# Kernel tuning notes

Hardware: AMD Instinct MI355X
Metric: run time of the kernel (lower is better)

Reference implementation:

```python
import jax, jax.numpy as jnp
import numpy as np

INPUT_DIM = 512
N_CLASSES = 100
N_SUBNETS = 20
HIDDEN = 32
WS1 = INPUT_DIM * HIDDEN   # 16384
BS1 = HIDDEN               # 32
WS2 = HIDDEN * N_CLASSES   # 3200
BS2 = N_CLASSES            # 100
TOTAL = WS1 + BS1 + WS2 + BS2  # 19716
LN_EPS = 1e-5


def _layernorm(v, g, b):
    mu = jnp.mean(v, axis=-1, keepdims=True)
    var = jnp.mean(jnp.square(v - mu), axis=-1, keepdims=True)
    return (v - mu) * jax.lax.rsqrt(var + LN_EPS) * g + b


def setup_inputs() -> dict:
    key = jax.random.key(0)
    ks = jax.random.split(key, 12)
    def lin(k, fan_in, shape):
        bound = 1.0 / np.sqrt(fan_in)
        return jax.random.uniform(k, shape, jnp.float32, -bound, bound)
    return {
        "x": jax.random.normal(ks[0], (32768, INPUT_DIM), jnp.float32),
        "W_h1": lin(ks[1], INPUT_DIM, (128, INPUT_DIM)),
        "b_h1": lin(ks[2], INPUT_DIM, (128,)),
        "g1": jnp.ones((128,), jnp.float32),
        "be1": jnp.zeros((128,), jnp.float32),
        "W_h2": lin(ks[3], 128, (256, 128)),
        "b_h2": lin(ks[4], 128, (256,)),
        "g2": jnp.ones((256,), jnp.float32),
        "be2": jnp.zeros((256,), jnp.float32),
        "W_h3": lin(ks[5], 256, (N_SUBNETS * TOTAL, 256)),
        "b_h3": lin(ks[6], 256, (N_SUBNETS * TOTAL,)),
        "ens_w": jnp.full((N_SUBNETS,), 1.0 / N_SUBNETS, jnp.float32),
    }


def reference(x, W_h1, b_h1, g1, be1, W_h2, b_h2, g2, be2, W_h3, b_h3, ens_w):
    # context from support set (= x itself): (1, input_dim)
    context = jnp.mean(x, axis=0, keepdims=True)
    # hypernet MLP (eval mode: dropout = identity)
    h = jax.nn.relu(_layernorm(context @ W_h1.T + b_h1, g1, be1))
    h = jax.nn.relu(_layernorm(h @ W_h2.T + b_h2, g2, be2))
    all_params = (h @ W_h3.T + b_h3).reshape(N_SUBNETS, TOTAL)
    # split generated params (same layout as torch .view)
    W1 = all_params[:, :WS1].reshape(N_SUBNETS, HIDDEN, INPUT_DIM)       # (S,H,I)
    b1 = all_params[:, WS1:WS1 + BS1]                                     # (S,H)
    W2 = all_params[:, WS1 + BS1:WS1 + BS1 + WS2].reshape(N_SUBNETS, N_CLASSES, HIDDEN)  # (S,C,H)
    b2 = all_params[:, WS1 + BS1 + WS2:]                                  # (S,C)
    # batched per-subnet 2-layer nets (dropout p=0.2 is identity in eval)
    hh = jax.nn.relu(jnp.einsum('bi,shi->sbh', x, W1) + b1[:, None, :])   # (S,B,H)
    logits = jnp.einsum('sbh,sch->sbc', hh, W2) + b2[:, None, :]          # (S,B,C)
    w = jax.nn.softmax(ens_w)                                             # (S,)
    return jnp.einsum('s,sbc->bc', w, logits)                             # (B,C)
```

## Files before the change

kernel.cpp:

```cpp
#include <hip/hip_runtime.h>
#include <hip/hip_bf16.h>

#define BATCH   32768
#define DIM     512
#define H1N     128
#define H2N     256
#define NSUB    20
#define HID     32
#define NCLS    100
#define NHID    640
#define TOTALP  19716
#define NPAR    394320
#define WS1P    16384
#define WS1B1   16416
#define WS2END  19616

#define OFF_PART 0
#define OFF_H    262144
#define OFF_W    262400
#define OFF_B1   262432
#define OFF_B2R  263072
#define OFF_W1B  265072
#define OFF_W2B  428912
#define OFF_XB   469872

typedef __attribute__((ext_vector_type(8))) short short8;
typedef __attribute__((ext_vector_type(4))) float f32x4;

static __device__ inline unsigned short f2bf(float f) {
    __hip_bfloat16 h = __float2bfloat16(f);
    return *reinterpret_cast<unsigned short*>(&h);
}

static __device__ __forceinline__ void gload16(const void* g, void* l) {
    __builtin_amdgcn_global_load_lds(
        (const __attribute__((address_space(1))) void*)g,
        (__attribute__((address_space(3))) void*)l, 16, 0, 0);
}

__global__ __launch_bounds__(256) void k1_colsum(const float* __restrict__ x,
                                                 float* __restrict__ F) {
    __shared__ float sP[DIM];
    int t = threadIdx.x, bid = blockIdx.x;
    int par = t >> 7;
    int c4 = (t & 127) * 4;
    const float* xb = x + (size_t)bid * 64 * DIM;
    unsigned short* ob = (unsigned short*)(F + OFF_XB) + (size_t)bid * 64 * DIM;
    float4 acc = make_float4(0.f, 0.f, 0.f, 0.f);
    #pragma unroll 8
    for (int i = 0; i < 32; ++i) {
        int r = 2 * i + par;
        float4 v = *(const float4*)(xb + r * DIM + c4);
        acc.x += v.x; acc.y += v.y; acc.z += v.z; acc.w += v.w;
        ushort4 u;
        u.x = f2bf(v.x); u.y = f2bf(v.y); u.z = f2bf(v.z); u.w = f2bf(v.w);
        *(ushort4*)(ob + r * DIM + c4) = u;
    }
    if (par == 0) *(float4*)(sP + c4) = acc;
    __syncthreads();
    if (par == 1) {
        float4 p = *(const float4*)(sP + c4);
        p.x += acc.x; p.y += acc.y; p.z += acc.z; p.w += acc.w;
        *(float4*)(F + OFF_PART + bid * DIM + c4) = p;
    }
}

__global__ __launch_bounds__(256) void k2_hyper(
    const float* __restrict__ Wh1, const float* __restrict__ bh1,
    const float* __restrict__ g1,  const float* __restrict__ be1,
    const float* __restrict__ Wh2, const float* __restrict__ bh2,
    const float* __restrict__ g2,  const float* __restrict__ be2,
    const float* __restrict__ ensw, float* __restrict__ F)
{
    __shared__ __align__(16) float sctx[DIM];
    __shared__ __align__(16) float sP2[DIM];
    __shared__ __align__(16) float sh1[H1N];
    __shared__ __align__(16) float sh2[H2N];
    int t = threadIdx.x;

    {
        int c4 = (t & 127) * 4;
        int half = t >> 7;
        float4 a = make_float4(0.f, 0.f, 0.f, 0.f);
        #pragma unroll 8
        for (int b = half * 256; b < half * 256 + 256; ++b) {
            float4 v = *(const float4*)(F + OFF_PART + b * DIM + c4);
            a.x += v.x; a.y += v.y; a.z += v.z; a.w += v.w;
        }
        if (half == 0) *(float4*)(sP2 + c4) = a;
        __syncthreads();
        if (half == 1) {
            float4 o = *(const float4*)(sP2 + c4);
            o.x = (o.x + a.x) * (1.0f / BATCH);
            o.y = (o.y + a.y) * (1.0f / BATCH);
            o.z = (o.z + a.z) * (1.0f / BATCH);
            o.w = (o.w + a.w) * (1.0f / BATCH);
            *(float4*)(sctx + c4) = o;
        }
        __syncthreads();
    }

    if (t < H1N) {
        float v = bh1[t];
        const float4* w = (const float4*)(Wh1 + t * DIM);
        for (int k = 0; k < DIM / 4; ++k) {
            float4 ww = w[k]; float4 c = *(const float4*)(sctx + k * 4);
            v += ww.x * c.x + ww.y * c.y + ww.z * c.z + ww.w * c.w;
        }
        sh1[t] = v;
    }
    __syncthreads();
    {
        float mu = 0.f;
        for (int k = 0; k < H1N; ++k) mu += sh1[k];
        mu *= (1.0f / H1N);
        float var = 0.f;
        for (int k = 0; k < H1N; ++k) { float d = sh1[k] - mu; var += d * d; }
        var *= (1.0f / H1N);
        float inv = rsqrtf(var + 1e-5f);
        __syncthreads();
        if (t < H1N) {
            float v = (sh1[t] - mu) * inv * g1[t] + be1[t];
            sh1[t] = fmaxf(v, 0.f);
        }
        __syncthreads();
    }

    {
        float v = bh2[t];
        const float4* w = (const float4*)(Wh2 + t * H1N);
        for (int k = 0; k < H1N / 4; ++k) {
            float4 ww = w[k]; float4 c = *(const float4*)(sh1 + k * 4);
            v += ww.x * c.x + ww.y * c.y + ww.z * c.z + ww.w * c.w;
        }
        sh2[t] = v;
    }
    __syncthreads();
    {
        float mu = 0.f;
        for (int k = 0; k < H2N; ++k) mu += sh2[k];
        mu *= (1.0f / H2N);
        float var = 0.f;
        for (int k = 0; k < H2N; ++k) { float d = sh2[k] - mu; var += d * d; }
        var *= (1.0f / H2N);
        float inv = rsqrtf(var + 1e-5f);
        float v = (sh2[t] - mu) * inv * g2[t] + be2[t];
        F[OFF_H + t] = fmaxf(v, 0.f);
    }

    if (t == 0) {
        float m = -1e30f;
        for (int s = 0; s < NSUB; ++s) m = fmaxf(m, ensw[s]);
        float sum = 0.f, e[NSUB];
        for (int s = 0; s < NSUB; ++s) { e[s] = __expf(ensw[s] - m); sum += e[s]; }
        for (int s = 0; s < NSUB; ++s) F[OFF_W + s] = e[s] / sum;
    }
}

static __device__ __forceinline__ void k3_pack(float* F, int row, float val) {
    __hip_bfloat16* W1B = (__hip_bfloat16*)(F + OFF_W1B);
    __hip_bfloat16* W2B = (__hip_bfloat16*)(F + OFF_W2B);
    int s = row / TOTALP;
    int r = row - s * TOTALP;
    if (r < WS1P) {
        int hh = r >> 9, k = r & 511;
        W1B[(s * HID + hh) * DIM + k] = __float2bfloat16(val);
    } else if (r < WS1B1) {
        F[OFF_B1 + s * HID + (r - WS1P)] = val;
    } else if (r < WS2END) {
        int q = r - WS1B1; int c = q >> 5, hh = q & 31;
        float ws = F[OFF_W + s];
        W2B[c * NHID + s * HID + hh] = __float2bfloat16(ws * val);
    } else {
        F[OFF_B2R + s * NCLS + (r - WS2END)] = val;
    }
}

__global__ __launch_bounds__(256) void k3_gemv(
    const float* __restrict__ Wh3, const float* __restrict__ bh3, float* __restrict__ F)
{
    int t = threadIdx.x;
    int wid = t >> 6, lane = t & 63;
    int row0 = blockIdx.x * 8 + wid * 2;
    const float4 h = *(const float4*)(F + OFF_H + lane * 4);
    const float4 w0 = *(const float4*)(Wh3 + (size_t)row0 * 256 + lane * 4);
    const float4 w1 = *(const float4*)(Wh3 + (size_t)(row0 + 1) * 256 + lane * 4);
    float d0 = w0.x * h.x + w0.y * h.y + w0.z * h.z + w0.w * h.w;
    float d1 = w1.x * h.x + w1.y * h.y + w1.z * h.z + w1.w * h.w;
    #pragma unroll
    for (int off = 32; off; off >>= 1) {
        d0 += __shfl_down(d0, off);
        d1 += __shfl_down(d1, off);
    }
    if (lane == 0) {
        k3_pack(F, row0,     d0 + bh3[row0]);
        k3_pack(F, row0 + 1, d1 + bh3[row0 + 1]);
    }
}

__global__ __launch_bounds__(256) void gemm_fused(
    const __hip_bfloat16* __restrict__ XB, const __hip_bfloat16* __restrict__ W1B,
    const __hip_bfloat16* __restrict__ W2B, const float* __restrict__ F,
    float* __restrict__ out)
{
    __shared__ __align__(16) unsigned char sA[64 * 256];
    __shared__ __align__(16) unsigned char sB[128 * 256];
    __shared__ __align__(16) unsigned char sP[64 * 256];
    const int t = threadIdx.x;
    int bid = blockIdx.x;
    const int cpx = gridDim.x >> 3;
    bid = (bid & 7) * cpx + (bid >> 3);
    const int Row0 = bid * 64;
    const int wid = t >> 6, lane = t & 63;
    const int l16 = lane & 15, lq = lane >> 4;

    f32x4 acc2[8];
    #pragma unroll
    for (int fn = 0; fn < 8; ++fn) acc2[fn] = (f32x4){0.f, 0.f, 0.f, 0.f};

    for (int n1 = 0; n1 < 5; ++n1) {
        f32x4 acc1[8];
        #pragma unroll
        for (int fn = 0; fn < 8; ++fn) acc1[fn] = (f32x4){0.f, 0.f, 0.f, 0.f};

        for (int kc = 0; kc < 512; kc += 128) {
            __syncthreads();
            #pragma unroll
            for (int i = 0; i < 4; ++i) {
                int ul = (wid * 4 + i) * 64 + lane;
                int row = ul >> 4, u = ul & 15;
                gload16(XB + (size_t)(Row0 + row) * 512 + kc + ((u ^ (row & 7)) << 3),
                        sA + (wid * 4 + i) * 1024);
            }
            #pragma unroll
            for (int i = 0; i < 8; ++i) {
                int ul = (wid * 8 + i) * 64 + lane;
                int row = ul >> 4, u = ul & 15;
                gload16(W1B + (size_t)(n1 * 128 + row) * 512 + kc + ((u ^ (row & 7)) << 3),
                        sB + (wid * 8 + i) * 1024);
            }
            __syncthreads();
            #pragma unroll
            for (int kk = 0; kk < 4; ++kk) {
                int u = kk * 4 + lq;
                int arow = wid * 16 + l16;
                short8 af = *(const short8*)(sA + arow * 256 + ((u ^ (arow & 7)) << 4));
                short8 bfv[8];
                #pragma unroll
                for (int fn = 0; fn < 8; ++fn) {
                    int rw = fn * 16 + l16;
                    bfv[fn] = *(const short8*)(sB + rw * 256 + ((u ^ (rw & 7)) << 4));
                }
                #pragma unroll
                for (int fn = 0; fn < 8; ++fn)
                    acc1[fn] = __builtin_amdgcn_mfma_f32_16x16x32_bf16(
                        af, bfv[fn], acc1[fn], 0, 0, 0);
            }
        }

        #pragma unroll
        for (int fn = 0; fn < 8; ++fn) {
            int col = fn * 16 + l16;
            float b1v = F[OFF_B1 + n1 * 128 + col];
            int unit = col >> 3;
            #pragma unroll
            for (int r = 0; r < 4; ++r) {
                int row = wid * 16 + lq * 4 + r;
                float v = fmaxf(acc1[fn][r] + b1v, 0.f);
                *(unsigned short*)(sP + row * 256 + ((unit ^ (row & 7)) << 4)
                                   + (col & 7) * 2) = f2bf(v);
            }
        }

        __syncthreads();
        #pragma unroll
        for (int i = 0; i < 8; ++i) {
            int ul = (wid * 8 + i) * 64 + lane;
            int row = ul >> 4, u = ul & 15;
            gload16(W2B + (size_t)row * NHID + n1 * 128 + ((u ^ (row & 7)) << 3),
                    sB + (wid * 8 + i) * 1024);
        }
        __syncthreads();
        #pragma unroll
        for (int kk = 0; kk < 4; ++kk) {
            int u = kk * 4 + lq;
            int arow = wid * 16 + l16;
            short8 af = *(const short8*)(sP + arow * 256 + ((u ^ (arow & 7)) << 4));
            short8 bfv[8];
            #pragma unroll
            for (int fn = 0; fn < 8; ++fn) {
                int rw = fn * 16 + l16;
                bfv[fn] = *(const short8*)(sB + rw * 256 + ((u ^ (rw & 7)) << 4));
            }
            #pragma unroll
            for (int fn = 0; fn < 8; ++fn)
                acc2[fn] = __builtin_amdgcn_mfma_f32_16x16x32_bf16(
                    af, bfv[fn], acc2[fn], 0, 0, 0);
        }
    }

    float* sBe = (float*)sA;
    __syncthreads();
    if (t < 128) {
        float b = 0.f;
        if (t < NCLS) {
            #pragma unroll
            for (int s = 0; s < NSUB; ++s)
                b += F[OFF_W + s] * F[OFF_B2R + s * NCLS + t];
        }
        sBe[t] = b;
    }
    __syncthreads();

    #pragma unroll
    for (int fn = 0; fn < 8; ++fn) {
        int gcol = fn * 16 + l16;
        if (gcol < NCLS) {
            float be = sBe[gcol];
            #pragma unroll
            for (int r = 0; r < 4; ++r) {
                int grow = Row0 + wid * 16 + lq * 4 + r;
                out[(size_t)grow * NCLS + gcol] = acc2[fn][r] + be;
            }
        }
    }
}

extern "C" void kernel_launch(void* const* d_in, const int* in_sizes, int n_in,
                              void* d_out, int out_size, void* d_ws, size_t ws_size,
                              hipStream_t stream)
{
    const float* x    = (const float*)d_in[0];
    const float* Wh1  = (const float*)d_in[1];
    const float* bh1  = (const float*)d_in[2];
    const float* g1   = (const float*)d_in[3];
    const float* be1  = (const float*)d_in[4];
    const float* Wh2  = (const float*)d_in[5];
    const float* bh2  = (const float*)d_in[6];
    const float* g2   = (const float*)d_in[7];
    const float* be2  = (const float*)d_in[8];
    const float* Wh3  = (const float*)d_in[9];
    const float* bh3  = (const float*)d_in[10];
    const float* ensw = (const float*)d_in[11];
    float* F = (float*)d_ws;
    float* out = (float*)d_out;

    const __hip_bfloat16* XB  = (const __hip_bfloat16*)(F + OFF_XB);
    const __hip_bfloat16* W1B = (const __hip_bfloat16*)(F + OFF_W1B);
    const __hip_bfloat16* W2B = (const __hip_bfloat16*)(F + OFF_W2B);

    k1_colsum<<<512, 256, 0, stream>>>(x, F);
    k2_hyper<<<1, 256, 0, stream>>>(Wh1, bh1, g1, be1, Wh2, bh2, g2, be2, ensw, F);
    k3_gemv<<<NPAR / 8, 256, 0, stream>>>(Wh3, bh3, F);
    gemm_fused<<<BATCH / 64, 256, 0, stream>>>(XB, W1B, W2B, F, out);
}
```

Before: 193.8 us.

## Double-buffer LDS tiles and switch to a 2x2 warp layout in the fused GEMM

Restructures the fused two-GEMM kernel into a flat 50-phase software pipeline. K-chunks are halved to 64 and the A/B LDS tiles are double-buffered, so the global loads for the next phase are issued while the current phase computes, with one barrier per phase instead of two. Warps are rearranged from a 4x1 layout (16 rows by 128 columns) to a 2x2 layout (32 rows by 64 columns), which cuts redundant B-fragment LDS reads per MFMA. In exchange it runs more, smaller phases with more control logic, and the per-phase lambda branches may add register pressure.

```diff
diff --git a/kernel.cpp b/kernel.cpp
--- a/kernel.cpp
+++ b/kernel.cpp
@@ -203,8 +203,8 @@
     const __hip_bfloat16* __restrict__ W2B, const float* __restrict__ F,
     float* __restrict__ out)
 {
-    __shared__ __align__(16) unsigned char sA[64 * 256];
-    __shared__ __align__(16) unsigned char sB[128 * 256];
+    __shared__ __align__(16) unsigned char sA[2][64 * 128];
+    __shared__ __align__(16) unsigned char sB[2][128 * 128];
     __shared__ __align__(16) unsigned char sP[64 * 256];
     const int t = threadIdx.x;
     int bid = blockIdx.x;
@@ -213,94 +213,140 @@
     const int Row0 = bid * 64;
     const int wid = t >> 6, lane = t & 63;
     const int l16 = lane & 15, lq = lane >> 4;
-
-    f32x4 acc2[8];
+    const int wr = wid >> 1, wc = wid & 1;
+
+    f32x4 acc1[2][4], acc2[2][4];
     #pragma unroll
-    for (int fn = 0; fn < 8; ++fn) acc2[fn] = (f32x4){0.f, 0.f, 0.f, 0.f};
-
-    for (int n1 = 0; n1 < 5; ++n1) {
-        f32x4 acc1[8];
+    for (int fm = 0; fm < 2; ++fm)
         #pragma unroll
-        for (int fn = 0; fn < 8; ++fn) acc1[fn] = (f32x4){0.f, 0.f, 0.f, 0.f};
-
-        for (int kc = 0; kc < 512; kc += 128) {
-            __syncthreads();
+        for (int fn = 0; fn < 4; ++fn)
+            acc2[fm][fn] = (f32x4){0.f, 0.f, 0.f, 0.f};
+
+    auto stage = [&](int p, int b) {
+        int n1 = p / 10, ph = p - n1 * 10;
+        if (ph < 8) {
+            int kc = ph * 64;
+            #pragma unroll
+            for (int i = 0; i < 2; ++i) {
+                int cidx = wid * 2 + i;
+                int ul = cidx * 64 + lane;
+                int row = ul >> 3, u = ul & 7;
+                gload16(XB + (size_t)(Row0 + row) * 512 + kc + ((u ^ (row & 7)) << 3),
+                        &sA[b][cidx * 1024]);
+            }
             #pragma unroll
             for (int i = 0; i < 4; ++i) {
-                int ul = (wid * 4 + i) * 64 + lane;
-                int row = ul >> 4, u = ul & 15;
-                gload16(XB + (size_t)(Row0 + row) * 512 + kc + ((u ^ (row & 7)) << 3),
-                        sA + (wid * 4 + i) * 1024);
-            }
-            #pragma unroll
-            for (int i = 0; i < 8; ++i) {
-                int ul = (wid * 8 + i) * 64 + lane;
-                int row = ul >> 4, u = ul & 15;
+                int cidx = wid * 4 + i;
+                int ul = cidx * 64 + lane;
+                int row = ul >> 3, u = ul & 7;
                 gload16(W1B + (size_t)(n1 * 128 + row) * 512 + kc + ((u ^ (row & 7)) << 3),
-                        sB + (wid * 8 + i) * 1024);
-            }
-            __syncthreads();
-            #pragma unroll
-            for (int kk = 0; kk < 4; ++kk) {
-                int u = kk * 4 + lq;
-                int arow = wid * 16 + l16;
-                short8 af = *(const short8*)(sA + arow * 256 + ((u ^ (arow & 7)) << 4));
-                short8 bfv[8];
-                #pragma unroll
-                for (int fn = 0; fn < 8; ++fn) {
-                    int rw = fn * 16 + l16;
-                    bfv[fn] = *(const short8*)(sB + rw * 256 + ((u ^ (rw & 7)) << 4));
-                }
-                #pragma unroll
-                for (int fn = 0; fn < 8; ++fn)
-                    acc1[fn] = __builtin_amdgcn_mfma_f32_16x16x32_bf16(
-                        af, bfv[fn], acc1[fn], 0, 0, 0);
-            }
-        }
-
+                        &sB[b][cidx * 1024]);
+            }
+        } else {
+            int h = ph - 8;
+            #pragma unroll
+            for (int i = 0; i < 4; ++i) {
+                int cidx = wid * 4 + i;
+                int ul = cidx * 64 + lane;
+                int row = ul >> 3, u = ul & 7;
+                gload16(W2B + (size_t)row * NHID + n1 * 128 + h * 64 + ((u ^ (row & 7)) << 3),
+                        &sB[b][cidx * 1024]);
+            }
+        }
+    };
+
+    auto compute = [&](int p, int b) {
+        int n1 = p / 10, ph = p - n1 * 10;
+        if (ph < 8) {
+            #pragma unroll
+            for (int kkl = 0; kkl < 2; ++kkl) {
+                int u = kkl * 4 + lq;
+                short8 af[2], bfv[4];
+                #pragma unroll
+                for (int fm = 0; fm < 2; ++fm) {
+                    int arow = wr * 32 + fm * 16 + l16;
+                    af[fm] = *(const short8*)(&sA[b][arow * 128 + ((u ^ (arow & 7)) << 4)]);
+                }
+                #pragma unroll
+                for (int fn = 0; fn < 4; ++fn) {
+                    int brow = wc * 64 + fn * 16 + l16;
+                    bfv[fn] = *(const short8*)(&sB[b][brow * 128 + ((u ^ (brow & 7)) << 4)]);
+                }
+                #pragma unroll
+                for (int fm = 0; fm < 2; ++fm)
+                    #pragma unroll
+                    for (int fn = 0; fn < 4; ++fn)
+                        acc1[fm][fn] = __builtin_amdgcn_mfma_f32_16x16x32_bf16(
+                            af[fm], bfv[fn], acc1[fm][fn], 0, 0, 0);
+            }
+        } else {
+            int h = ph - 8;
+            #pragma unroll
+            for (int kkl = 0; kkl < 2; ++kkl) {
+                int u = kkl * 4 + lq;
+                int punit = (h * 2 + kkl) * 4 + lq;
+                short8 af[2], bfv[4];
+                #pragma unroll
+                for (int fm = 0; fm < 2; ++fm) {
+                    int prow = wr * 32 + fm * 16 + l16;
+                    af[fm] = *(const short8*)(&sP[prow * 256 + ((punit ^ (prow & 7)) << 4)]);
+                }
+                #pragma unroll
+                for (int fn = 0; fn < 4; ++fn) {
+                    int brow = wc * 64 + fn * 16 + l16;
+                    bfv[fn] = *(const short8*)(&sB[b][brow * 128 + ((u ^ (brow & 7)) << 4)]);
+                }
+                #pragma unroll
+                for (int fm = 0; fm < 2; ++fm)
+                    #pragma unroll
+                    for (int fn = 0; fn < 4; ++fn)
+                        acc2[fm][fn] = __builtin_amdgcn_mfma_f32_16x16x32_bf16(
+                            af[fm], bfv[fn], acc2[fm][fn], 0, 0, 0);
+            }
+        }
+    };
+
+    auto pack = [&](int n1) {
         #pragma unroll
-        for (int fn = 0; fn < 8; ++fn) {
-            int col = fn * 16 + l16;
-            float b1v = F[OFF_B1 + n1 * 128 + col];
-            int unit = col >> 3;
-            #pragma unroll
-            for (int r = 0; r < 4; ++r) {
-                int row = wid * 16 + lq * 4 + r;
-                float v = fmaxf(acc1[fn][r] + b1v, 0.f);
-                *(unsigned short*)(sP + row * 256 + ((unit ^ (row & 7)) << 4)
-                                   + (col & 7) * 2) = f2bf(v);
-            }
-        }
-
+        for (int fm = 0; fm < 2; ++fm) {
+            #pragma unroll
+            for (int fn = 0; fn < 4; ++fn) {
+                int col = wc * 64 + fn * 16 + l16;
+                float b1v = F[OFF_B1 + n1 * 128 + col];
+                int unit = col >> 3;
+                #pragma unroll
+                for (int r = 0; r < 4; ++r) {
+                    int row = wr * 32 + fm * 16 + lq * 4 + r;
+                    float v = fmaxf(acc1[fm][fn][r] + b1v, 0.f);
+                    *(unsigned short*)(&sP[row * 256 + ((unit ^ (row & 7)) << 4)
+                                       + (col & 7) * 2]) = f2bf(v);
+                }
+            }
+        }
+    };
+
+    stage(0, 0);
+    __syncthreads();
+    int buf = 0;
+    for (int p = 0; p < 49; ++p) {
+        stage(p + 1, buf ^ 1);
+        int ph = p % 10;
+        if (ph == 0) {
+            #pragma unroll
+            for (int fm = 0; fm < 2; ++fm)
+                #pragma unroll
+                for (int fn = 0; fn < 4; ++fn)
+                    acc1[fm][fn] = (f32x4){0.f, 0.f, 0.f, 0.f};
+        }
+        compute(p, buf);
+        if (ph == 7) pack(p / 10);
         __syncthreads();
-        #pragma unroll
-        for (int i = 0; i < 8; ++i) {
-            int ul = (wid * 8 + i) * 64 + lane;
-            int row = ul >> 4, u = ul & 15;
-            gload16(W2B + (size_t)row * NHID + n1 * 128 + ((u ^ (row & 7)) << 3),
-                    sB + (wid * 8 + i) * 1024);
-        }
-        __syncthreads();
-        #pragma unroll
-        for (int kk = 0; kk < 4; ++kk) {
-            int u = kk * 4 + lq;
-            int arow = wid * 16 + l16;
-            short8 af = *(const short8*)(sP + arow * 256 + ((u ^ (arow & 7)) << 4));
-            short8 bfv[8];
-            #pragma unroll
-            for (int fn = 0; fn < 8; ++fn) {
-                int rw = fn * 16 + l16;
-                bfv[fn] = *(const short8*)(sB + rw * 256 + ((u ^ (rw & 7)) << 4));
-            }
-            #pragma unroll
-            for (int fn = 0; fn < 8; ++fn)
-                acc2[fn] = __builtin_amdgcn_mfma_f32_16x16x32_bf16(
-                    af, bfv[fn], acc2[fn], 0, 0, 0);
-        }
-    }
-
-    float* sBe = (float*)sA;
-    __syncthreads();
+        buf ^= 1;
+    }
+    compute(49, buf);
+    __syncthreads();
+
+    float* sBe = (float*)&sA[0][0];
     if (t < 128) {
         float b = 0.f;
         if (t < NCLS) {
@@ -313,14 +359,17 @@
     __syncthreads();
 
     #pragma unroll
-    for (int fn = 0; fn < 8; ++fn) {
-        int gcol = fn * 16 + l16;
-        if (gcol < NCLS) {
-            float be = sBe[gcol];
-            #pragma unroll
-            for (int r = 0; r < 4; ++r) {
-                int grow = Row0 + wid * 16 + lq * 4 + r;
-                out[(size_t)grow * NCLS + gcol] = acc2[fn][r] + be;
+    for (int fm = 0; fm < 2; ++fm) {
+        #pragma unroll
+        for (int fn = 0; fn < 4; ++fn) {
+            int gcol = wc * 64 + fn * 16 + l16;
+            if (gcol < NCLS) {
+                float be = sBe[gcol];
+                #pragma unroll
+                for (int r = 0; r < 4; ++r) {
+                    int grow = Row0 + wr * 32 + fm * 16 + lq * 4 + r;
+                    out[(size_t)grow * NCLS + gcol] = acc2[fm][fn][r] + be;
+                }
             }
         }
     }
```

After: 202.1 us. +4.2%, slower.

## Double-buffer LDS tiles with async prefetch pipeline across both GEMM stages

Applied to the files above, without the earlier changes.

Restructures the fused two-GEMM kernel into a 10-step-per-chunk software pipeline. K-tiles shrink to 64 and the LDS buffers for X, W1 and W2 are double-buffered, so global loads for the next step are issued before computing on the current one. Explicit vmcnt waits and raw barriers replace the paired __syncthreads. This hides global-to-LDS latency behind MFMA work, at the cost of more barriers per chunk and fragile hand-counted waitcnt values.

```diff
diff --git a/kernel.cpp b/kernel.cpp
--- a/kernel.cpp
+++ b/kernel.cpp
@@ -203,8 +203,8 @@
     const __hip_bfloat16* __restrict__ W2B, const float* __restrict__ F,
     float* __restrict__ out)
 {
-    __shared__ __align__(16) unsigned char sA[64 * 256];
-    __shared__ __align__(16) unsigned char sB[128 * 256];
+    __shared__ __align__(16) unsigned char sA[2][64 * 128];
+    __shared__ __align__(16) unsigned char sB[2][128 * 128];
     __shared__ __align__(16) unsigned char sP[64 * 256];
     const int t = threadIdx.x;
     int bid = blockIdx.x;
@@ -214,93 +214,130 @@
     const int wid = t >> 6, lane = t & 63;
     const int l16 = lane & 15, lq = lane >> 4;
 
-    f32x4 acc2[8];
+    f32x4 acc1[8], acc2[8];
     #pragma unroll
     for (int fn = 0; fn < 8; ++fn) acc2[fn] = (f32x4){0.f, 0.f, 0.f, 0.f};
 
-    for (int n1 = 0; n1 < 5; ++n1) {
-        f32x4 acc1[8];
-        #pragma unroll
-        for (int fn = 0; fn < 8; ++fn) acc1[fn] = (f32x4){0.f, 0.f, 0.f, 0.f};
-
-        for (int kc = 0; kc < 512; kc += 128) {
-            __syncthreads();
-            #pragma unroll
-            for (int i = 0; i < 4; ++i) {
-                int ul = (wid * 4 + i) * 64 + lane;
-                int row = ul >> 4, u = ul & 15;
-                gload16(XB + (size_t)(Row0 + row) * 512 + kc + ((u ^ (row & 7)) << 3),
-                        sA + (wid * 4 + i) * 1024);
-            }
-            #pragma unroll
-            for (int i = 0; i < 8; ++i) {
-                int ul = (wid * 8 + i) * 64 + lane;
-                int row = ul >> 4, u = ul & 15;
-                gload16(W1B + (size_t)(n1 * 128 + row) * 512 + kc + ((u ^ (row & 7)) << 3),
-                        sB + (wid * 8 + i) * 1024);
-            }
-            __syncthreads();
-            #pragma unroll
-            for (int kk = 0; kk < 4; ++kk) {
-                int u = kk * 4 + lq;
-                int arow = wid * 16 + l16;
-                short8 af = *(const short8*)(sA + arow * 256 + ((u ^ (arow & 7)) << 4));
-                short8 bfv[8];
-                #pragma unroll
-                for (int fn = 0; fn < 8; ++fn) {
-                    int rw = fn * 16 + l16;
-                    bfv[fn] = *(const short8*)(sB + rw * 256 + ((u ^ (rw & 7)) << 4));
-                }
-                #pragma unroll
-                for (int fn = 0; fn < 8; ++fn)
-                    acc1[fn] = __builtin_amdgcn_mfma_f32_16x16x32_bf16(
-                        af, bfv[fn], acc1[fn], 0, 0, 0);
-            }
-        }
-
-        #pragma unroll
-        for (int fn = 0; fn < 8; ++fn) {
-            int col = fn * 16 + l16;
-            float b1v = F[OFF_B1 + n1 * 128 + col];
-            int unit = col >> 3;
-            #pragma unroll
-            for (int r = 0; r < 4; ++r) {
-                int row = wid * 16 + lq * 4 + r;
-                float v = fmaxf(acc1[fn][r] + b1v, 0.f);
-                *(unsigned short*)(sP + row * 256 + ((unit ^ (row & 7)) << 4)
-                                   + (col & 7) * 2) = f2bf(v);
-            }
-        }
-
-        __syncthreads();
-        #pragma unroll
-        for (int i = 0; i < 8; ++i) {
-            int ul = (wid * 8 + i) * 64 + lane;
-            int row = ul >> 4, u = ul & 15;
-            gload16(W2B + (size_t)row * NHID + n1 * 128 + ((u ^ (row & 7)) << 3),
-                    sB + (wid * 8 + i) * 1024);
-        }
-        __syncthreads();
-        #pragma unroll
-        for (int kk = 0; kk < 4; ++kk) {
+    auto stage1 = [&](int n1, int kc, int b) {
+        #pragma unroll
+        for (int i = 0; i < 2; ++i) {
+            int cidx = wid * 2 + i;
+            int ul = cidx * 64 + lane;
+            int row = ul >> 3, u = ul & 7;
+            gload16(XB + (size_t)(Row0 + row) * 512 + kc + ((u ^ (row & 7)) << 3),
+                    &sA[b][cidx * 1024]);
+        }
+        #pragma unroll
+        for (int i = 0; i < 4; ++i) {
+            int cidx = wid * 4 + i;
+            int ul = cidx * 64 + lane;
+            int row = ul >> 3, u = ul & 7;
+            gload16(W1B + (size_t)(n1 * 128 + row) * 512 + kc + ((u ^ (row & 7)) << 3),
+                    &sB[b][cidx * 1024]);
+        }
+    };
+    auto stageW2 = [&](int n1, int h, int b) {
+        #pragma unroll
+        for (int i = 0; i < 4; ++i) {
+            int cidx = wid * 4 + i;
+            int ul = cidx * 64 + lane;
+            int row = ul >> 3, u = ul & 7;
+            gload16(W2B + (size_t)row * NHID + n1 * 128 + h * 64 + ((u ^ (row & 7)) << 3),
+                    &sB[b][cidx * 1024]);
+        }
+    };
+    auto comp1 = [&](int b) {
+        #pragma unroll
+        for (int kk = 0; kk < 2; ++kk) {
             int u = kk * 4 + lq;
             int arow = wid * 16 + l16;
-            short8 af = *(const short8*)(sP + arow * 256 + ((u ^ (arow & 7)) << 4));
+            short8 af = *(const short8*)(&sA[b][arow * 128 + ((u ^ (arow & 7)) << 4)]);
             short8 bfv[8];
             #pragma unroll
             for (int fn = 0; fn < 8; ++fn) {
                 int rw = fn * 16 + l16;
-                bfv[fn] = *(const short8*)(sB + rw * 256 + ((u ^ (rw & 7)) << 4));
+                bfv[fn] = *(const short8*)(&sB[b][rw * 128 + ((u ^ (rw & 7)) << 4)]);
+            }
+            #pragma unroll
+            for (int fn = 0; fn < 8; ++fn)
+                acc1[fn] = __builtin_amdgcn_mfma_f32_16x16x32_bf16(
+                    af, bfv[fn], acc1[fn], 0, 0, 0);
+        }
+    };
+    auto comp2 = [&](int h, int b) {
+        #pragma unroll
+        for (int kk = 0; kk < 2; ++kk) {
+            int u = kk * 4 + lq;
+            int punit = (h * 2 + kk) * 4 + lq;
+            int arow = wid * 16 + l16;
+            short8 af = *(const short8*)(&sP[arow * 256 + ((punit ^ (arow & 7)) << 4)]);
+            short8 bfv[8];
+            #pragma unroll
+            for (int fn = 0; fn < 8; ++fn) {
+                int rw = fn * 16 + l16;
+                bfv[fn] = *(const short8*)(&sB[b][rw * 128 + ((u ^ (rw & 7)) << 4)]);
             }
             #pragma unroll
             for (int fn = 0; fn < 8; ++fn)
                 acc2[fn] = __builtin_amdgcn_mfma_f32_16x16x32_bf16(
                     af, bfv[fn], acc2[fn], 0, 0, 0);
         }
-    }
-
-    float* sBe = (float*)sA;
-    __syncthreads();
+    };
+
+    int buf = 0;
+    stage1(0, 0, 0);
+    float b1r[8];
+
+    for (int n1 = 0; n1 < 5; ++n1) {
+        #pragma unroll
+        for (int st = 0; st < 10; ++st) {
+            if (st < 9) {
+                if (st + 1 < 8) stage1(n1, (st + 1) * 64, buf ^ 1);
+                else stageW2(n1, st + 1 - 8, buf ^ 1);
+            } else if (n1 < 4) {
+                stage1(n1 + 1, 0, buf ^ 1);
+            }
+            if (st < 9) {
+                if (st + 1 < 8) asm volatile("s_waitcnt vmcnt(6)" ::: "memory");
+                else            asm volatile("s_waitcnt vmcnt(4)" ::: "memory");
+            } else if (n1 < 4) {
+                asm volatile("s_waitcnt vmcnt(6)" ::: "memory");
+            } else {
+                asm volatile("s_waitcnt vmcnt(0)" ::: "memory");
+            }
+            __builtin_amdgcn_s_barrier();
+            __builtin_amdgcn_sched_barrier(0);
+
+            if (st == 0) {
+                #pragma unroll
+                for (int fn = 0; fn < 8; ++fn) {
+                    acc1[fn] = (f32x4){0.f, 0.f, 0.f, 0.f};
+                    b1r[fn] = F[OFF_B1 + n1 * 128 + fn * 16 + l16];
+                }
+            }
+            if (st < 8) comp1(buf);
+            else comp2(st - 8, buf);
+            if (st == 7) {
+                #pragma unroll
+                for (int fn = 0; fn < 8; ++fn) {
+                    int col = fn * 16 + l16;
+                    int unit = col >> 3;
+                    #pragma unroll
+                    for (int r = 0; r < 4; ++r) {
+                        int row = wid * 16 + lq * 4 + r;
+                        float v = fmaxf(acc1[fn][r] + b1r[fn], 0.f);
+                        *(unsigned short*)(&sP[row * 256 + ((unit ^ (row & 7)) << 4)
+                                           + (col & 7) * 2]) = f2bf(v);
+                    }
+                }
+            }
+            __builtin_amdgcn_sched_barrier(0);
+            __builtin_amdgcn_s_barrier();
+            buf ^= 1;
+        }
+    }
+
+    float* sBe = (float*)&sA[0][0];
     if (t < 128) {
         float b = 0.f;
         if (t < NCLS) {
```

Measured after the change: 192.6 us. About the same (-0.6%).
